# Kernel tuning notes

Measured on AMD Instinct MI355X. Metric: run time of the kernel, lower is better.

## Reference

```python
import jax, jax.numpy as jnp
import numpy as np


def setup_inputs() -> dict:
    key = jax.random.key(0)
    k1, k2, k3 = jax.random.split(key, 3)
    N, K, C, M = 16, 32768, 16, 128
    pred_boxes = jax.random.normal(k1, (N, K, 5), dtype=jnp.float32)
    pred_cls = jax.random.normal(k2, (N, K, C), dtype=jnp.float32)
    target = jax.random.uniform(k3, (N, M, 5), dtype=jnp.float32)
    return {"pred_boxes": pred_boxes, "pred_cls": pred_cls, "target": target}


def _losses(pred_boxes, pred_cls, target):
    N, K, _ = pred_boxes.shape
    M = target.shape[1]
    C = pred_cls.shape[2]
    mask = target.sum(axis=2) != 0                      # (N, M)
    maskf = mask.astype(pred_boxes.dtype)
    denom = maskf.sum()
    tboxes = target[..., 1:]                            # (N, M, 4) corners (x1,y1,x2,y2)
    tcls = target[..., 0].astype(jnp.int32)             # (N, M)
    pconf = pred_boxes[..., 4]                          # (N, K)
    pb = pred_boxes[..., :4]                            # (N, K, 4) (x, y, w, h)

    # pred corners (N, 1, K)
    p_x1 = pb[:, None, :, 0]
    p_y1 = pb[:, None, :, 1]
    p_x2 = (pb[..., 2] + pb[..., 0])[:, None, :]
    p_y2 = (pb[..., 3] + pb[..., 1])[:, None, :]
    # target corners (N, M, 1)
    t_x1 = tboxes[..., 0:1]
    t_y1 = tboxes[..., 1:2]
    t_x2 = tboxes[..., 2:3]
    t_y2 = tboxes[..., 3:4]

    ix1 = jnp.maximum(p_x1, t_x1)
    iy1 = jnp.maximum(p_y1, t_y1)
    ix2 = jnp.minimum(p_x2, t_x2)
    iy2 = jnp.minimum(p_y2, t_y2)
    inter = jnp.clip(ix2 - ix1 + 1, 0) * jnp.clip(iy2 - iy1 + 1, 0)   # (N, M, K)
    a1 = (p_x2 - p_x1 + 1) * (p_y2 - p_y1 + 1)
    a2 = (t_x2 - t_x1 + 1) * (t_y2 - t_y1 + 1)
    iou = inter / (a1 + a2 - inter + 1e-16)

    best = jnp.argmax(iou, axis=-1)                     # (N, M)
    best_idx = jnp.where(mask, best, 0)                 # masked targets keep index 0 (as torch init)

    best_pb = jnp.take_along_axis(pb, best_idx[..., None], axis=1)       # (N, M, 4)
    best_cls = jnp.take_along_axis(pred_cls, best_idx[..., None], axis=1)  # (N, M, C)
    # NOTE: faithful to original: conf gather indices are never updated -> always index 0
    conf_idx = jnp.zeros((N, M), dtype=jnp.int32)
    best_conf = jax.nn.sigmoid(jnp.take_along_axis(pconf, conf_idx, axis=1))  # (N, M)

    def masked_mean(v):
        return (v * maskf).sum() / denom

    logp = jax.nn.log_softmax(best_cls, axis=-1)
    ce = -jnp.take_along_axis(logp, tcls[..., None], axis=-1)[..., 0]
    loss_cls = masked_mean(ce)

    loss_x = masked_mean((best_pb[..., 0] - tboxes[..., 0]) ** 2)
    loss_y = masked_mean((best_pb[..., 1] - tboxes[..., 1]) ** 2)
    loss_w = masked_mean((best_pb[..., 2] - (tboxes[..., 2] - tboxes[..., 0])) ** 2)
    loss_h = masked_mean((best_pb[..., 3] - (tboxes[..., 3] - tboxes[..., 1])) ** 2)

    labels = (best_conf > 0.5).astype(best_conf.dtype)
    bce = -(labels * jnp.log(best_conf) + (1.0 - labels) * jnp.log(1.0 - best_conf))
    loss_conf = masked_mean(bce)

    loss = loss_cls + loss_x + loss_y + loss_w + loss_h + loss_conf
    return loss, loss_cls, loss_x, loss_y, loss_w, loss_h, loss_conf


def reference(pred_boxes, pred_cls, target):
    return _losses(pred_boxes, pred_cls, target)
```

## Files before the change

### kernel.cpp

```cpp
#include <hip/hip_runtime.h>
#include <math.h>

constexpr int N_ = 16;
constexpr int K_ = 32768;
constexpr int C_ = 16;
constexpr int M_ = 128;

constexpr int KC = 512;
constexpr int CHUNKS = K_ / KC;
constexpr int WAVES = 8;
constexpr int GROUPS = 16;

#define POISON_U 0xAAAAAAAAu

__device__ __forceinline__ unsigned long long load_agent_u64(
    const unsigned long long* p) {
  return __hip_atomic_load(p, __ATOMIC_RELAXED, __HIP_MEMORY_SCOPE_AGENT);
}
__device__ __forceinline__ void store_agent_f32(float* p, float v) {
  __hip_atomic_store(p, v, __ATOMIC_RELAXED, __HIP_MEMORY_SCOPE_AGENT);
}
__device__ __forceinline__ float load_agent_f32(const float* p) {
  return __hip_atomic_load(p, __ATOMIC_RELAXED, __HIP_MEMORY_SCOPE_AGENT);
}

__global__ __launch_bounds__(512, 8) void fused_loss_kernel(
    const float* __restrict__ pred_boxes,
    const float* __restrict__ pred_cls,
    const float* __restrict__ target,
    unsigned long long* __restrict__ rowmin,
    float* __restrict__ ws2,
    int* __restrict__ cnt,
    float* __restrict__ out) {
  __shared__ float4 lds4[KC];
  __shared__ float ldsa1[KC];
  __shared__ int key_s[WAVES][M_];
  __shared__ float red[WAVES][7];
  __shared__ int s_flag;

  const int chunk = blockIdx.x;
  const int n = blockIdx.y;
  const int k0 = chunk * KC;
  const int tid = threadIdx.x;

  {
    const float* p = pred_boxes + ((size_t)(n * K_ + k0 + tid)) * 5;
    const float x = p[0];
    const float y = p[1];
    const float bw = p[2];
    const float bh = p[3];
    const float px2 = bw + x;
    const float py2 = bh + y;
    lds4[tid] = make_float4(x, y, px2 + 1.0f, py2 + 1.0f);
    ldsa1[tid] = (px2 - x + 1.0f) * (py2 - y + 1.0f);
  }
  __syncthreads();

  const int wv = tid >> 6;
  const int lane = tid & 63;
  const int rb = lane & 31;
  const int half = (lane >> 5) & 1;
  const int ks = (wv * 2 + half) * 32;
  const int hbase = ((1 - half) << 5) | 31;

  float tx1[4], ty1[4], tx2[4], ty2[4], a2[4];
#pragma unroll
  for (int j = 0; j < 4; ++j) {
    const float* tg = target + ((size_t)(n * M_ + rb + 32 * j)) * 5;
    tx1[j] = tg[1];
    ty1[j] = tg[2];
    tx2[j] = tg[3] + 1.0f;
    ty2[j] = tg[4] + 1.0f;
    a2[j] = (tg[3] - tg[1] + 1.0f) * (tg[4] - tg[2] + 1.0f) + 1e-16f;
  }

  int best[4];
#pragma unroll
  for (int j = 0; j < 4; ++j) best[j] = (int)0x80000000;

#pragma unroll 8
  for (int kl = 0; kl < 32; ++kl) {
    const float4 v = lds4[ks + kl];
    const float a1 = ldsa1[ks + kl];
    const unsigned idx6 = (unsigned)(hbase - kl);
#pragma unroll
    for (int j = 0; j < 4; ++j) {
      float ww = fminf(v.z, tx2[j]) - fmaxf(v.x, tx1[j]);
      float hh = fminf(v.w, ty2[j]) - fmaxf(v.y, ty1[j]);
      ww = fmaxf(ww, 0.0f);
      hh = fmaxf(hh, 0.0f);
      const float inter = ww * hh;
      const float iou = inter * __builtin_amdgcn_rcpf((a1 + a2[j]) - inter);
      const int key = (int)((__float_as_uint(iou) & 0xFFFFFE00u) | idx6);
      best[j] = best[j] > key ? best[j] : key;
    }
  }

#pragma unroll
  for (int j = 0; j < 4; ++j) {
    const int other = __shfl_xor(best[j], 32, 64);
    best[j] = best[j] > other ? best[j] : other;
  }
  if (lane < 32) {
    const unsigned wvf = (unsigned)(7 - wv) << 6;
#pragma unroll
    for (int j = 0; j < 4; ++j) {
      const unsigned u = (unsigned)best[j];
      key_s[wv][rb + 32 * j] = (int)((u & 0xFFFFFE00u) | wvf | (u & 63u));
    }
  }
  __syncthreads();

  if (tid < M_) {
    int mg = key_s[0][tid];
#pragma unroll
    for (int w2 = 1; w2 < WAVES; ++w2) {
      const int v = key_s[w2][tid];
      mg = mg > v ? mg : v;
    }
    const unsigned e = (unsigned)mg & 511u;
    const int gk = k0 + (511 - (int)e);
    const unsigned tr = (unsigned)mg & 0xFFFFFE00u;
    const unsigned ord = tr ^ (unsigned)(((int)tr >> 31) | 0x80000000);
    const int grp = chunk & (GROUPS - 1);
    atomicMin(&rowmin[((size_t)grp * N_ + n) * M_ + tid],
              ((unsigned long long)(~ord) << 32) | (unsigned)gk);
  }

  __syncthreads();
  if (tid == 0) {
    const unsigned old = (unsigned)atomicAdd(&cnt[n], 1);
    s_flag = (old == POISON_U + (CHUNKS - 1)) || (old == CHUNKS - 1);
  }
  __syncthreads();
  if (!s_flag) return;

  {
    const int m = tid & (M_ - 1);
    float acc[7] = {0, 0, 0, 0, 0, 0, 0};
    if (tid < M_) {
      unsigned long long bestk = ~0ull;
#pragma unroll
      for (int g = 0; g < GROUPS; ++g) {
        const unsigned long long pk =
            load_agent_u64(&rowmin[((size_t)g * N_ + n) * M_ + m]);
        bestk = pk < bestk ? pk : bestk;
      }
      const int bidx0 = (int)(unsigned)bestk;

      const float* tg2 = target + ((size_t)(n * M_ + m)) * 5;
      const float t0 = tg2[0], t1 = tg2[1], t2 = tg2[2], t3 = tg2[3],
                  t4 = tg2[4];
      const float sum5 = t0 + t1 + t2 + t3 + t4;
      const float mk = (sum5 != 0.0f) ? 1.0f : 0.0f;
      const int bidx = (sum5 != 0.0f) ? bidx0 : 0;

      const float* pb = pred_boxes + ((size_t)(n * K_ + bidx)) * 5;
      const float b0 = pb[0], b1 = pb[1], bw = pb[2], bh = pb[3];

      const float4* pc =
          (const float4*)(pred_cls + ((size_t)(n * K_ + bidx)) * C_);
      float vals[C_];
#pragma unroll
      for (int q = 0; q < 4; ++q) {
        const float4 vv = pc[q];
        vals[q * 4 + 0] = vv.x;
        vals[q * 4 + 1] = vv.y;
        vals[q * 4 + 2] = vv.z;
        vals[q * 4 + 3] = vv.w;
      }
      int tcls = (int)t0;
      tcls = tcls < 0 ? 0 : (tcls >= C_ ? C_ - 1 : tcls);
      float mx = -INFINITY;
#pragma unroll
      for (int q = 0; q < C_; ++q) mx = fmaxf(mx, vals[q]);
      float se = 0.0f;
#pragma unroll
      for (int q = 0; q < C_; ++q) se += expf(vals[q] - mx);
      const float ce2 = logf(se) + mx - vals[tcls];

      const float dx = b0 - t1;
      const float dy = b1 - t2;
      const float dw = bw - (t3 - t1);
      const float dh = bh - (t4 - t2);

      const float pcf = pred_boxes[(size_t)n * K_ * 5 + 4];
      const float bc = 1.0f / (1.0f + expf(-pcf));
      const float bce = (bc > 0.5f) ? -logf(bc) : -logf(1.0f - bc);

      acc[0] = mk;
      acc[1] = mk * ce2;
      acc[2] = mk * dx * dx;
      acc[3] = mk * dy * dy;
      acc[4] = mk * dw * dw;
      acc[5] = mk * dh * dh;
      acc[6] = mk * bce;
    }

#pragma unroll
    for (int i = 0; i < 7; ++i) {
      float v = acc[i];
      for (int off = 32; off > 0; off >>= 1) v += __shfl_down(v, off, 64);
      acc[i] = v;
    }
    const int lane2 = tid & 63;
    const int wid = tid >> 6;
    if (lane2 == 0) {
#pragma unroll
      for (int i = 0; i < 7; ++i) red[wid][i] = acc[i];
    }
    __syncthreads();

    if (tid == 0) {
      float sum7[7];
#pragma unroll
      for (int i = 0; i < 7; ++i) {
        float s = 0.0f;
#pragma unroll
        for (int w2 = 0; w2 < WAVES; ++w2) s += red[w2][i];
        sum7[i] = s;
      }
#pragma unroll
      for (int i = 0; i < 7; ++i) store_agent_f32(&ws2[n * 8 + i], sum7[i]);
    }
    __syncthreads();
    if (tid == 0) {
      const unsigned old2 = (unsigned)atomicAdd(&cnt[N_], 1);
      s_flag = (old2 == POISON_U + (N_ - 1)) || (old2 == N_ - 1);
    }
    __syncthreads();
  }

  if (s_flag && tid == 0) {
    float s[7] = {0, 0, 0, 0, 0, 0, 0};
    for (int nn = 0; nn < N_; ++nn)
#pragma unroll
      for (int i = 0; i < 7; ++i) s[i] += load_agent_f32(&ws2[nn * 8 + i]);
    const float denom = s[0];
    const float lc = s[1] / denom;
    const float lx = s[2] / denom;
    const float ly = s[3] / denom;
    const float lw = s[4] / denom;
    const float lh = s[5] / denom;
    const float lf = s[6] / denom;
    out[0] = lc + lx + ly + lw + lh + lf;
    out[1] = lc;
    out[2] = lx;
    out[3] = ly;
    out[4] = lw;
    out[5] = lh;
    out[6] = lf;
  }
}

extern "C" void kernel_launch(void* const* d_in, const int* in_sizes, int n_in,
                              void* d_out, int out_size, void* d_ws, size_t ws_size,
                              hipStream_t stream) {
  const float* pred_boxes = (const float*)d_in[0];
  const float* pred_cls = (const float*)d_in[1];
  const float* target = (const float*)d_in[2];
  float* out = (float*)d_out;

  unsigned long long* rowmin = (unsigned long long*)d_ws;
  float* ws2 = (float*)(rowmin + (size_t)GROUPS * N_ * M_);
  int* cnt = (int*)(ws2 + N_ * 8);

  dim3 g(CHUNKS, N_);
  fused_loss_kernel<<<g, 512, 0, stream>>>(pred_boxes, pred_cls, target,
                                           rowmin, ws2, cnt, out);
}
```

Baseline: 115.3 us.

## Process two chunks per block and replace grouped atomicMin with per-block slot stores

Each block now handles two 512-wide K chunks in sequence, which halves the grid and the per-block target loads. Instead of atomicMin into 16 grouped accumulators, each block writes its best key to a dedicated slot, and the last block per image reduces all 32 slots. This removes atomic contention and the need for the rowmin buffer to start at ~0. In exchange it halves parallelism, adds extra barriers inside the chunk loop, and lowers the launch-bounds occupancy hint from 8 to 4.

```diff
diff --git a/kernel.cpp b/kernel.cpp
--- a/kernel.cpp
+++ b/kernel.cpp
@@ -7,9 +7,9 @@
 constexpr int M_ = 128;
 
 constexpr int KC = 512;
-constexpr int CHUNKS = K_ / KC;
+constexpr int CPB = 2;
+constexpr int CPW = K_ / (KC * CPB);
 constexpr int WAVES = 8;
-constexpr int GROUPS = 16;
 
 #define POISON_U 0xAAAAAAAAu
 
@@ -17,6 +17,10 @@
     const unsigned long long* p) {
   return __hip_atomic_load(p, __ATOMIC_RELAXED, __HIP_MEMORY_SCOPE_AGENT);
 }
+__device__ __forceinline__ void store_agent_u64(unsigned long long* p,
+                                                unsigned long long v) {
+  __hip_atomic_store(p, v, __ATOMIC_RELAXED, __HIP_MEMORY_SCOPE_AGENT);
+}
 __device__ __forceinline__ void store_agent_f32(float* p, float v) {
   __hip_atomic_store(p, v, __ATOMIC_RELAXED, __HIP_MEMORY_SCOPE_AGENT);
 }
@@ -24,37 +28,23 @@
   return __hip_atomic_load(p, __ATOMIC_RELAXED, __HIP_MEMORY_SCOPE_AGENT);
 }
 
-__global__ __launch_bounds__(512, 8) void fused_loss_kernel(
+__global__ __launch_bounds__(512, 4) void fused_loss_kernel(
     const float* __restrict__ pred_boxes,
     const float* __restrict__ pred_cls,
     const float* __restrict__ target,
-    unsigned long long* __restrict__ rowmin,
+    unsigned long long* __restrict__ rowwin,
     float* __restrict__ ws2,
     int* __restrict__ cnt,
     float* __restrict__ out) {
   __shared__ float4 lds4[KC];
   __shared__ float ldsa1[KC];
-  __shared__ int key_s[WAVES][M_];
+  __shared__ int key_s[WAVES][CPB][M_];
   __shared__ float red[WAVES][7];
   __shared__ int s_flag;
 
-  const int chunk = blockIdx.x;
+  const int bx = blockIdx.x;
   const int n = blockIdx.y;
-  const int k0 = chunk * KC;
   const int tid = threadIdx.x;
-
-  {
-    const float* p = pred_boxes + ((size_t)(n * K_ + k0 + tid)) * 5;
-    const float x = p[0];
-    const float y = p[1];
-    const float bw = p[2];
-    const float bh = p[3];
-    const float px2 = bw + x;
-    const float py2 = bh + y;
-    lds4[tid] = make_float4(x, y, px2 + 1.0f, py2 + 1.0f);
-    ldsa1[tid] = (px2 - x + 1.0f) * (py2 - y + 1.0f);
-  }
-  __syncthreads();
 
   const int wv = tid >> 6;
   const int lane = tid & 63;
@@ -74,63 +64,85 @@
     a2[j] = (tg[3] - tg[1] + 1.0f) * (tg[4] - tg[2] + 1.0f) + 1e-16f;
   }
 
-  int best[4];
-#pragma unroll
-  for (int j = 0; j < 4; ++j) best[j] = (int)0x80000000;
+  for (int cc = 0; cc < CPB; ++cc) {
+    const int k0 = (bx * CPB + cc) * KC;
+
+    {
+      const float* p = pred_boxes + ((size_t)(n * K_ + k0 + tid)) * 5;
+      const float x = p[0];
+      const float y = p[1];
+      const float bw = p[2];
+      const float bh = p[3];
+      const float px2 = bw + x;
+      const float py2 = bh + y;
+      lds4[tid] = make_float4(x, y, px2 + 1.0f, py2 + 1.0f);
+      ldsa1[tid] = (px2 - x + 1.0f) * (py2 - y + 1.0f);
+    }
+    __syncthreads();
+
+    int best[4];
+#pragma unroll
+    for (int j = 0; j < 4; ++j) best[j] = (int)0x80000000;
 
 #pragma unroll 8
-  for (int kl = 0; kl < 32; ++kl) {
-    const float4 v = lds4[ks + kl];
-    const float a1 = ldsa1[ks + kl];
-    const unsigned idx6 = (unsigned)(hbase - kl);
+    for (int kl = 0; kl < 32; ++kl) {
+      const float4 v = lds4[ks + kl];
+      const float a1 = ldsa1[ks + kl];
+      const unsigned idx6 = (unsigned)(hbase - kl);
+#pragma unroll
+      for (int j = 0; j < 4; ++j) {
+        float ww = fminf(v.z, tx2[j]) - fmaxf(v.x, tx1[j]);
+        float hh = fminf(v.w, ty2[j]) - fmaxf(v.y, ty1[j]);
+        ww = fmaxf(ww, 0.0f);
+        hh = fmaxf(hh, 0.0f);
+        const float inter = ww * hh;
+        const float iou = inter * __builtin_amdgcn_rcpf((a1 + a2[j]) - inter);
+        const int key = (int)((__float_as_uint(iou) & 0xFFFFFE00u) | idx6);
+        best[j] = best[j] > key ? best[j] : key;
+      }
+    }
+
 #pragma unroll
     for (int j = 0; j < 4; ++j) {
-      float ww = fminf(v.z, tx2[j]) - fmaxf(v.x, tx1[j]);
-      float hh = fminf(v.w, ty2[j]) - fmaxf(v.y, ty1[j]);
-      ww = fmaxf(ww, 0.0f);
-      hh = fmaxf(hh, 0.0f);
-      const float inter = ww * hh;
-      const float iou = inter * __builtin_amdgcn_rcpf((a1 + a2[j]) - inter);
-      const int key = (int)((__float_as_uint(iou) & 0xFFFFFE00u) | idx6);
-      best[j] = best[j] > key ? best[j] : key;
-    }
-  }
-
-#pragma unroll
-  for (int j = 0; j < 4; ++j) {
-    const int other = __shfl_xor(best[j], 32, 64);
-    best[j] = best[j] > other ? best[j] : other;
-  }
-  if (lane < 32) {
-    const unsigned wvf = (unsigned)(7 - wv) << 6;
-#pragma unroll
-    for (int j = 0; j < 4; ++j) {
-      const unsigned u = (unsigned)best[j];
-      key_s[wv][rb + 32 * j] = (int)((u & 0xFFFFFE00u) | wvf | (u & 63u));
-    }
-  }
-  __syncthreads();
+      const int other = __shfl_xor(best[j], 32, 64);
+      best[j] = best[j] > other ? best[j] : other;
+    }
+    if (lane < 32) {
+      const unsigned wvf = (unsigned)(7 - wv) << 6;
+#pragma unroll
+      for (int j = 0; j < 4; ++j) {
+        const unsigned u = (unsigned)best[j];
+        key_s[wv][cc][rb + 32 * j] = (int)((u & 0xFFFFFE00u) | wvf | (u & 63u));
+      }
+    }
+    __syncthreads();
+  }
 
   if (tid < M_) {
-    int mg = key_s[0][tid];
-#pragma unroll
-    for (int w2 = 1; w2 < WAVES; ++w2) {
-      const int v = key_s[w2][tid];
-      mg = mg > v ? mg : v;
-    }
-    const unsigned e = (unsigned)mg & 511u;
-    const int gk = k0 + (511 - (int)e);
-    const unsigned tr = (unsigned)mg & 0xFFFFFE00u;
-    const unsigned ord = tr ^ (unsigned)(((int)tr >> 31) | 0x80000000);
-    const int grp = chunk & (GROUPS - 1);
-    atomicMin(&rowmin[((size_t)grp * N_ + n) * M_ + tid],
-              ((unsigned long long)(~ord) << 32) | (unsigned)gk);
+    unsigned long long bestu = ~0ull;
+#pragma unroll
+    for (int cc = 0; cc < CPB; ++cc) {
+      int mg = key_s[0][cc][tid];
+#pragma unroll
+      for (int w2 = 1; w2 < WAVES; ++w2) {
+        const int v = key_s[w2][cc][tid];
+        mg = mg > v ? mg : v;
+      }
+      const unsigned e = (unsigned)mg & 511u;
+      const int gk = (bx * CPB + cc) * KC + (511 - (int)e);
+      const unsigned tr = (unsigned)mg & 0xFFFFFE00u;
+      const unsigned ord = tr ^ (unsigned)(((int)tr >> 31) | 0x80000000);
+      const unsigned long long u =
+          ((unsigned long long)(~ord) << 32) | (unsigned)gk;
+      bestu = u < bestu ? u : bestu;
+    }
+    store_agent_u64(&rowwin[((size_t)n * CPW + bx) * M_ + tid], bestu);
   }
 
   __syncthreads();
   if (tid == 0) {
     const unsigned old = (unsigned)atomicAdd(&cnt[n], 1);
-    s_flag = (old == POISON_U + (CHUNKS - 1)) || (old == CHUNKS - 1);
+    s_flag = (old == POISON_U + (CPW - 1)) || (old == CPW - 1);
   }
   __syncthreads();
   if (!s_flag) return;
@@ -141,9 +153,9 @@
     if (tid < M_) {
       unsigned long long bestk = ~0ull;
 #pragma unroll
-      for (int g = 0; g < GROUPS; ++g) {
+      for (int g = 0; g < CPW; ++g) {
         const unsigned long long pk =
-            load_agent_u64(&rowmin[((size_t)g * N_ + n) * M_ + m]);
+            load_agent_u64(&rowwin[((size_t)n * CPW + g) * M_ + m]);
         bestk = pk < bestk ? pk : bestk;
       }
       const int bidx0 = (int)(unsigned)bestk;
@@ -261,11 +273,11 @@
   const float* target = (const float*)d_in[2];
   float* out = (float*)d_out;
 
-  unsigned long long* rowmin = (unsigned long long*)d_ws;
-  float* ws2 = (float*)(rowmin + (size_t)GROUPS * N_ * M_);
+  unsigned long long* rowwin = (unsigned long long*)d_ws;
+  float* ws2 = (float*)(rowwin + (size_t)N_ * CPW * M_);
   int* cnt = (int*)(ws2 + N_ * 8);
 
-  dim3 g(CHUNKS, N_);
+  dim3 g(CPW, N_);
   fused_loss_kernel<<<g, 512, 0, stream>>>(pred_boxes, pred_cls, target,
-                                           rowmin, ws2, cnt, out);
-}
+                                           rowwin, ws2, cnt, out);
+}
```

Result: no change. 116.5 us (+1.0%).
